# Optimization experiments

Measured on AMD Instinct MI355X. Metric: run time of the kernel, lower is better.

## Reference

```python
import jax, jax.numpy as jnp
import numpy as np
from jax import lax

B, T, V = 128, 256, 64
HF = 32   # MLP feature-imputation hidden
CTX = 32  # context hidden
HID = 64  # LSTM hidden


def _uniform(k, shape, fan):
    s = 1.0 / np.sqrt(fan)
    return jax.random.uniform(k, shape, jnp.float32, -s, s)


def setup_inputs():
    key = jax.random.key(0)
    ks = jax.random.split(key, 40)
    values = jax.random.normal(ks[0], (B, T, V), jnp.float32)
    masks = (jax.random.uniform(ks[1], (B, T, V)) > 0.3).astype(jnp.float32)
    deltas = jax.random.uniform(ks[2], (B, T, V), jnp.float32) * 5.0
    lengths = jax.random.randint(ks[3], (B,), T // 2, T + 1)
    min_vals = jnp.min(values, axis=1, keepdims=True)
    max_vals = jnp.max(values, axis=1, keepdims=True)
    D_in = 2 * V + 2 * CTX
    return dict(
        lengths=lengths, values=values, masks=masks, deltas=deltas,
        min_vals=min_vals, max_vals=max_vals,
        W_decay=_uniform(ks[4], (V, V), V), b_decay=_uniform(ks[5], (V,), V),
        W_feat=_uniform(ks[6], (V, HF, V), V), b_feat=_uniform(ks[7], (V, HF), V),
        W_nl1=_uniform(ks[8], (HF, HF), HF), b_nl1=_uniform(ks[9], (HF,), HF),
        W_nl2=_uniform(ks[10], (1, HF), HF), b_nl2=_uniform(ks[11], (1,), HF),
        Wc1=_uniform(ks[12], (2 * CTX, 3 * V + 1), 3 * V + 1), bc1=_uniform(ks[13], (2 * CTX,), 3 * V + 1),
        Wc2=_uniform(ks[14], (CTX, 2 * CTX), 2 * CTX), bc2=_uniform(ks[15], (CTX,), 2 * CTX),
        W_ih_g=_uniform(ks[16], (3 * CTX, 2 * V), CTX), W_hh_g=_uniform(ks[17], (3 * CTX, CTX), CTX),
        b_ih_g=_uniform(ks[18], (3 * CTX,), CTX), b_hh_g=_uniform(ks[19], (3 * CTX,), CTX),
        W_init=_uniform(ks[20], (2 * HID, 2 * CTX), 2 * CTX), b_init=_uniform(ks[21], (2 * HID,), 2 * CTX),
        W_ih_f=_uniform(ks[22], (4 * HID, D_in), HID), W_hh_f=_uniform(ks[23], (4 * HID, HID), HID),
        b_ih_f=_uniform(ks[24], (4 * HID,), HID), b_hh_f=_uniform(ks[25], (4 * HID,), HID),
        W_ih_b=_uniform(ks[26], (4 * HID, D_in), HID), W_hh_b=_uniform(ks[27], (4 * HID, HID), HID),
        b_ih_b=_uniform(ks[28], (4 * HID,), HID), b_hh_b=_uniform(ks[29], (4 * HID,), HID),
        W_ri=_uniform(ks[30], (V, 2 * HID), 2 * HID), b_ri=_uniform(ks[31], (V,), 2 * HID),
        W_fu=_uniform(ks[32], (V, 2 * V), 2 * V), b_fu=_uniform(ks[33], (V,), 2 * V),
    )


def _gru(x, h, Wih, Whh, bih, bhh):
    gi = x @ Wih.T + bih
    gh = h @ Whh.T + bhh
    ir, iz, inn = jnp.split(gi, 3, axis=-1)
    hr, hz, hn = jnp.split(gh, 3, axis=-1)
    r = jax.nn.sigmoid(ir + hr)
    z = jax.nn.sigmoid(iz + hz)
    n = jnp.tanh(inn + r * hn)
    return (1.0 - z) * n + z * h


def _lstm(x, h, c, Wih, Whh, bih, bhh):
    g = x @ Wih.T + bih + h @ Whh.T + bhh
    i, f, gg, o = jnp.split(g, 4, axis=-1)
    c = jax.nn.sigmoid(f) * c + jax.nn.sigmoid(i) * jnp.tanh(gg)
    h = jax.nn.sigmoid(o) * jnp.tanh(c)
    return h, c


def _forward(lengths, values, masks, deltas, min_vals, max_vals,
             W_decay, b_decay, W_feat, b_feat, W_nl1, b_nl1, W_nl2, b_nl2,
             Wc1, bc1, Wc2, bc2, W_ih_g, W_hh_g, b_ih_g, b_hh_g,
             W_init, b_init, W_ih_f, W_hh_f, b_ih_f, b_hh_f,
             W_ih_b, W_hh_b, b_ih_b, b_hh_b, W_ri, b_ri, W_fu, b_fu):
    Bb, Tt, Vv = values.shape
    lf = lengths.astype(jnp.float32)
    pad = (jnp.arange(Tt)[None, :] + 1 <= lengths[:, None]).astype(jnp.float32)  # [B,T]

    msum = masks.sum(axis=1)                       # [B,V] observation counts
    means = values.sum(axis=1) / msum
    var = ((values - means[:, None, :]) ** 2).sum(axis=1) / (msum - 1.0)
    stdev = jnp.sqrt(var)
    missing = 1.0 - msum / lf[:, None]
    stats = jnp.concatenate([lf[:, None], means, stdev, missing], axis=1)  # [B,3V+1]

    mmn = jnp.maximum(max_vals - min_vals, 1e-8)   # [B,1,V]
    nv = (values - min_vals) / mmn
    nmeans = (means - min_vals[:, 0, :]) / mmn[:, 0, :]

    # last-observation-carried-forward x_prime
    nv_tm = jnp.swapaxes(nv, 0, 1)   # [T,B,V]
    m_tm = jnp.swapaxes(masks, 0, 1)

    def pstep(xp, xm):
        x_prev, m_prev = xm
        xp = m_prev * x_prev + (1.0 - m_prev) * xp
        return xp, xp
    _, xp_rest = lax.scan(pstep, nv_tm[0], (nv_tm[:-1], m_tm[:-1]))
    x_prime = jnp.swapaxes(jnp.concatenate([nv_tm[:1], xp_rest], axis=0), 0, 1)

    # InputTemporalDecay: F.linear(d, W*I, b) == d * diag(W) + b
    gamma = jnp.exp(-jax.nn.relu(deltas * jnp.diag(W_decay) + b_decay))
    x_decay = gamma * x_prime + (1.0 - gamma) * nmeans[:, None, :]
    x_complete = masks * nv + (1.0 - masks) * x_decay

    # context vectors
    ctx_mlp = jax.nn.relu(stats @ Wc1.T + bc1) @ Wc2.T + bc2  # [B,CTX]
    x_rnn_tm = jnp.swapaxes(jnp.concatenate([x_complete, masks], axis=-1), 0, 1)  # [T,B,2V]
    pad_tm = jnp.swapaxes(pad, 0, 1)[:, :, None]
    h0 = jnp.zeros((Bb, W_hh_g.shape[1]), values.dtype)

    def gstep(carry, inp):
        h, hn = carry
        x_t, p_t = inp
        h = _gru(x_t, h, W_ih_g, W_hh_g, b_ih_g, b_hh_g)
        hn = p_t * h + (1.0 - p_t) * hn
        return (h, hn), None
    (_, ctx_rnn), _ = lax.scan(gstep, (h0, h0), (x_rnn_tm, pad_tm))
    context = jnp.concatenate([ctx_mlp, ctx_rnn], axis=1)  # [B,2*CTX]

    hinit = context @ W_init.T + b_init  # [B,2H]
    cinit = jnp.tanh(hinit)
    Hh = hinit.shape[1] // 2
    hf0, hb0 = hinit[:, :Hh], hinit[:, Hh:]
    cf0, cb0 = cinit[:, :Hh], cinit[:, Hh:]

    ctx_bt = jnp.broadcast_to(context[:, None, :], (Bb, Tt, context.shape[1]))
    rnn_in_tm = jnp.swapaxes(jnp.concatenate([x_complete, masks, ctx_bt], axis=-1), 0, 1)  # [T,B,D]

    def fstep(carry, x):
        h, c = _lstm(x, carry[0], carry[1], W_ih_f, W_hh_f, b_ih_f, b_hh_f)
        return (h, c), h
    _, hf_rest = lax.scan(fstep, (hf0, cf0), rnn_in_tm[:-1])
    hf_all = jnp.concatenate([hf0[None], hf_rest], axis=0)  # [T,B,H]

    def bstep(carry, x):
        h, c = _lstm(x, carry[0], carry[1], W_ih_b, W_hh_b, b_ih_b, b_hh_b)
        return (h, c), h
    _, hb_rest = lax.scan(bstep, (hb0, cb0), rnn_in_tm[1:][::-1])  # t = T-1 .. 1
    hb_all = jnp.concatenate([hb0[None], hb_rest], axis=0)[::-1]   # time-aligned

    h_cat = jnp.concatenate([hf_all, hb_all], axis=-1)  # [T,B,2H]
    rnn_imp = jnp.swapaxes(h_cat @ W_ri.T + b_ri, 0, 1)  # [B,T,V]

    # per-variable masked feature imputation (no self-connection)
    eye = jnp.eye(Vv, dtype=values.dtype)
    Wm = W_feat * (1.0 - eye[:, None, :])                 # [V,HF,V]
    hidden = jnp.einsum('btv,ghv->btgh', x_complete, Wm) + b_feat  # [B,T,V,HF]
    z = jax.nn.relu(hidden) @ W_nl1.T + b_nl1
    feat_imp = (jax.nn.relu(z) @ W_nl2.T + b_nl2)[..., 0]  # [B,T,V]

    beta = jax.nn.sigmoid(jnp.concatenate([gamma, masks], axis=-1) @ W_fu.T + b_fu)
    final_imp = beta * feat_imp + (1.0 - beta) * rnn_imp

    # unnormalize all three estimates; stack as [3,B,T,V]
    out = jnp.stack([rnn_imp, feat_imp, final_imp], axis=0) * mmn[None] + min_vals[None]
    return out


def reference(lengths, values, masks, deltas, min_vals, max_vals,
              W_decay, b_decay, W_feat, b_feat, W_nl1, b_nl1, W_nl2, b_nl2,
              Wc1, bc1, Wc2, bc2, W_ih_g, W_hh_g, b_ih_g, b_hh_g,
              W_init, b_init, W_ih_f, W_hh_f, b_ih_f, b_hh_f,
              W_ih_b, W_hh_b, b_ih_b, b_hh_b, W_ri, b_ri, W_fu, b_fu):
    return _forward(lengths, values, masks, deltas, min_vals, max_vals,
                    W_decay, b_decay, W_feat, b_feat, W_nl1, b_nl1, W_nl2, b_nl2,
                    Wc1, bc1, Wc2, bc2, W_ih_g, W_hh_g, b_ih_g, b_hh_g,
                    W_init, b_init, W_ih_f, W_hh_f, b_ih_f, b_hh_f,
                    W_ih_b, W_hh_b, b_ih_b, b_hh_b, W_ri, b_ri, W_fu, b_fu)
```

## Files before the change

### kernel.cpp

```cpp
#include <hip/hip_runtime.h>
#include <hip/hip_fp16.h>

static constexpr int NB = 128;
static constexpr int NT = 256;
static constexpr int NV = 64;
static constexpr int NBT = NB * NT;
static constexpr int NBTV = NBT * NV;

typedef __attribute__((ext_vector_type(8))) short short8;
typedef __attribute__((ext_vector_type(4))) float f32x4;
typedef __attribute__((ext_vector_type(4))) float fvec4;

__device__ __forceinline__ void wave_lds_fence() {
    __builtin_amdgcn_sched_barrier(0);
    asm volatile("s_waitcnt lgkmcnt(0)" ::: "memory");
    __builtin_amdgcn_sched_barrier(0);
}

__device__ __forceinline__ void block_sync_lds() {
    __builtin_amdgcn_sched_barrier(0);
    asm volatile("s_waitcnt lgkmcnt(0)" ::: "memory");
    __builtin_amdgcn_s_barrier();
    asm volatile("" ::: "memory");
    __builtin_amdgcn_sched_barrier(0);
}

__device__ __forceinline__ unsigned short f2bf(float x) {
    unsigned int u = __float_as_uint(x);
    return (unsigned short)((u + 0x7FFFu + ((u >> 16) & 1u)) >> 16);
}
__device__ __forceinline__ float bf2f(unsigned short b) {
    return __uint_as_float(((unsigned int)b) << 16);
}
__device__ __forceinline__ unsigned short f2h(float x) {
    union { _Float16 h; unsigned short u; } c; c.h = (_Float16)x; return c.u;
}
__device__ __forceinline__ float fsigm(float x) {
    return __builtin_amdgcn_rcpf(1.0f + __expf(-x));
}
__device__ __forceinline__ float ftanh(float x) {
    return 1.0f - 2.0f * __builtin_amdgcn_rcpf(1.0f + __expf(2.0f * x));
}

__device__ __forceinline__ short8 pack8(float4 a, float4 b) {
    short8 r;
    r[0] = (short)f2bf(a.x); r[1] = (short)f2bf(a.y); r[2] = (short)f2bf(a.z); r[3] = (short)f2bf(a.w);
    r[4] = (short)f2bf(b.x); r[5] = (short)f2bf(b.y); r[6] = (short)f2bf(b.z); r[7] = (short)f2bf(b.w);
    return r;
}

__device__ __forceinline__ void dot4(float4& acc, const float4 wv, const float4 xv) {
    acc.x = fmaf(wv.x, xv.x, acc.x);
    acc.y = fmaf(wv.y, xv.y, acc.y);
    acc.z = fmaf(wv.z, xv.z, acc.z);
    acc.w = fmaf(wv.w, xv.w, acc.w);
}

__global__ __launch_bounds__(256) void k_prep(
    const float* __restrict__ Wf, const float* __restrict__ Wihf,
    const float* __restrict__ Wihb, const float* __restrict__ Wihg,
    const float* __restrict__ Whhf, const float* __restrict__ Whhb,
    const float* __restrict__ Whhg, const float* __restrict__ Wri,
    const float* __restrict__ Wfu,
    unsigned short* __restrict__ wbf, float* __restrict__ wdiag,
    unsigned short* __restrict__ wgf, unsigned short* __restrict__ wgb,
    unsigned short* __restrict__ wgg,
    unsigned short* __restrict__ whhf_h, unsigned short* __restrict__ whhb_h,
    unsigned short* __restrict__ whhg_h,
    unsigned short* __restrict__ wri_bf, unsigned short* __restrict__ wfu_bf,
    const int* __restrict__ lengths, const float* __restrict__ values,
    const float* __restrict__ masks, const float* __restrict__ minv,
    const float* __restrict__ maxv, float* __restrict__ stats,
    float* __restrict__ mmn_ws, float* __restrict__ nmeans_ws) {
    __shared__ float red[3][4][64];
    int bx = blockIdx.x;
    if (bx < 512) {
        int i = bx * 256 + threadIdx.x;
        if (i < NV * 32 * NV) wbf[i] = f2bf(Wf[i]);
        if (i < 2048) wdiag[i] = bf2f(f2bf(Wf[i * 64 + (i >> 5)]));
        if (i < 32768) {
            int n = i >> 7, k = i & 127;
            wgf[i] = f2bf(Wihf[n * 192 + k]);
            wgb[i] = f2bf(Wihb[n * 192 + k]);
        }
        if (i < 12288) wgg[i] = f2bf(Wihg[i]);
        if (i < 16384) { whhf_h[i] = f2h(Whhf[i]); whhb_h[i] = f2h(Whhb[i]); }
        if (i < 3072) whhg_h[i] = f2h(Whhg[i]);
        if (i < 8192) { wri_bf[i] = f2bf(Wri[i]); wfu_bf[i] = f2bf(Wfu[i]); }
    } else {
        int b = bx - 512; int tid = threadIdx.x;
        int v = tid & 63; int tc = tid >> 6;
        const float* vp = values + (size_t)b * NT * NV;
        const float* mp = masks + (size_t)b * NT * NV;
        float sv = 0.f, sq = 0.f, sm = 0.f;
        for (int t = tc; t < NT; t += 4) {
            float x = vp[t * NV + v]; float m = mp[t * NV + v];
            sv += x; sq += x * x; sm += m;
        }
        red[0][tc][v] = sv; red[1][tc][v] = sq; red[2][tc][v] = sm;
        __syncthreads();
        if (tc == 0) {
            sv = red[0][0][v] + red[0][1][v] + red[0][2][v] + red[0][3][v];
            sq = red[1][0][v] + red[1][1][v] + red[1][2][v] + red[1][3][v];
            sm = red[2][0][v] + red[2][1][v] + red[2][2][v] + red[2][3][v];
            float mean = sv / sm;
            float var = (sq - 2.0f * mean * sv + (float)NT * mean * mean) / (sm - 1.0f);
            var = fmaxf(var, 0.0f);
            float sd = sqrtf(var);
            float lf = (float)lengths[b];
            float miss = 1.0f - sm / lf;
            float mn = minv[b * NV + v]; float mx = maxv[b * NV + v];
            float mm = fmaxf(mx - mn, 1e-8f);
            float* st = stats + b * 256;
            if (v == 0) st[0] = lf;
            st[1 + v] = mean; st[65 + v] = sd; st[129 + v] = miss;
            mmn_ws[b * NV + v] = mm;
            nmeans_ws[b * NV + v] = (mean - mn) / mm;
        }
    }
}

__global__ __launch_bounds__(256) void k_fill(
    const float* __restrict__ values, const float* __restrict__ masks,
    const float* __restrict__ deltas, const float* __restrict__ minv,
    const float* __restrict__ Wd, const float* __restrict__ bd,
    const float* __restrict__ mmn_ws, const float* __restrict__ nmeans_ws,
    float* __restrict__ xcomp, float* __restrict__ gam) {
    int b = blockIdx.x; int tid = threadIdx.x;
    int v = tid & 63; int tc = tid >> 6;
    float mn = minv[b * NV + v];
    float mm = mmn_ws[b * NV + v];
    float nmean = nmeans_ws[b * NV + v];
    float wd = Wd[v * NV + v], bdv = bd[v];
    size_t base = (size_t)b * NT * NV + v;
    __shared__ float lastv[4][64];
    __shared__ int hasf[4][64];
    __shared__ float nv0s[64];
    int t0 = tc * 64;
    float last = 0.f; int has = 0;
    for (int t = t0; t < t0 + 64; t++) {
        float val = values[base + (size_t)t * NV];
        float m = masks[base + (size_t)t * NV];
        float nv = (val - mn) / mm;
        if (m != 0.f) { last = nv; has = 1; }
        if (tc == 0 && t == 0) nv0s[v] = nv;
    }
    lastv[tc][v] = last; hasf[tc][v] = has;
    __syncthreads();
    float xp = nv0s[v];
    for (int q = tc - 1; q >= 0; q--) {
        if (hasf[q][v]) { xp = lastv[q][v]; break; }
    }
    for (int t = t0; t < t0 + 64; t++) {
        size_t i = base + (size_t)t * NV;
        float val = values[i], m = masks[i], d = deltas[i];
        float nv = (val - mn) / mm;
        float g = expf(-fmaxf(fmaf(d, wd, bdv), 0.0f));
        float xd = g * xp + (1.0f - g) * nmean;
        float xc = m * nv + (1.0f - m) * xd;
        xcomp[i] = xc; gam[i] = g;
        xp = (m != 0.f) ? nv : xp;
    }
}

__global__ __launch_bounds__(256) void k_gates_g(
    const float* __restrict__ xcomp, const float* __restrict__ masks,
    const unsigned short* __restrict__ wgg, const float* __restrict__ bihg,
    float* __restrict__ gg) {
    int wave = threadIdx.x >> 6, lane = threadIdx.x & 63;
    int bt0 = blockIdx.x * 64 + wave * 16;
    int r = lane & 15, kc = lane >> 4;
    const float* xr = xcomp + (size_t)(bt0 + r) * NV + kc * 8;
    const float* mr = masks + (size_t)(bt0 + r) * NV + kc * 8;
    short8 af0 = pack8(*(const float4*)(xr), *(const float4*)(xr + 4));
    short8 af1 = pack8(*(const float4*)(xr + 32), *(const float4*)(xr + 36));
    short8 af2 = pack8(*(const float4*)(mr), *(const float4*)(mr + 4));
    short8 af3 = pack8(*(const float4*)(mr + 32), *(const float4*)(mr + 36));
    #pragma unroll 3
    for (int nt = 0; nt < 6; nt++) {
        const unsigned short* w = wgg + (size_t)(nt * 16 + r) * 128 + kc * 8;
        float bias = bihg[nt * 16 + r];
        f32x4 acc = {bias, bias, bias, bias};
        acc = __builtin_amdgcn_mfma_f32_16x16x32_bf16(af0, *(const short8*)(w), acc, 0, 0, 0);
        acc = __builtin_amdgcn_mfma_f32_16x16x32_bf16(af1, *(const short8*)(w + 32), acc, 0, 0, 0);
        acc = __builtin_amdgcn_mfma_f32_16x16x32_bf16(af2, *(const short8*)(w + 64), acc, 0, 0, 0);
        acc = __builtin_amdgcn_mfma_f32_16x16x32_bf16(af3, *(const short8*)(w + 96), acc, 0, 0, 0);
        #pragma unroll
        for (int i = 0; i < 4; i++)
            gg[(size_t)(bt0 + kc * 4 + i) * 96 + nt * 16 + r] = acc[i];
    }
}

#define GRU_STEP(T, GIN) { \
    const int t_ = (T); const int p_ = t_ & 1; \
    int4 raw_[4]; \
    const int4* hp_ = (const int4*)hsg[g][s]; \
    _Pragma("unroll") for (int q = 0; q < 4; q++) raw_[q] = hp_[q]; \
    const __half2* hhv_ = (const __half2*)raw_; \
    __half2 a0_ = zh2, a1_ = zh2, a2_ = zh2, a3_ = zh2; \
    _Pragma("unroll") for (int q = 0; q < 16; q += 4) { \
        a0_ = __hfma2(w2[q],     hhv_[q],     a0_); \
        a1_ = __hfma2(w2[q + 1], hhv_[q + 1], a1_); \
        a2_ = __hfma2(w2[q + 2], hhv_[q + 2], a2_); \
        a3_ = __hfma2(w2[q + 3], hhv_[q + 3], a3_); } \
    __half2 sA_ = __hadd2(__hadd2(a0_, a1_), __hadd2(a2_, a3_)); \
    float d_ = __low2float(sA_) + __high2float(sA_); \
    if (g < 2) { \
        gexg[p_][s][n][g] = GIN + bh + d_; \
    } else { \
        gexg[p_][s][n][2] = bh + d_; \
        gexg[p_][s][n][3] = GIN; \
    } \
    block_sync_lds(); \
    float qx_ = gexg[p_][s][n][0], qy_ = gexg[p_][s][n][1]; \
    float qz_ = gexg[p_][s][n][2], qw_ = gexg[p_][s][n][3]; \
    float rr_ = fsigm(qx_); \
    float zz_ = fsigm(qy_); \
    float nn_ = ftanh(qw_ + rr_ * qz_); \
    float h_ = (1.f - zz_) * nn_ + zz_ * hprev; \
    hprev = h_; \
    if (t_ < len) hn = h_; \
    hsg[g][s][n] = f2h(h_); \
    wave_lds_fence(); \
}

#define FEAT_BODY(BT0) { \
    int bt0 = (BT0); \
    int r = lane & 15, kc = lane >> 4; \
    unsigned short* hbw = hbs[wave]; \
    float* lx = ldsx[wave]; \
    float* flw = fls[wave]; \
    short8 a0, a1; \
    { \
        const float* xr = xcomp + (size_t)(bt0 + r) * NV + kc * 8; \
        a0 = pack8(*(const float4*)(xr), *(const float4*)(xr + 4)); \
        a1 = pack8(*(const float4*)(xr + 32), *(const float4*)(xr + 36)); \
    } \
    { \
        int gc0 = kc * 16; \
        const float* xr2 = xcomp + (size_t)(bt0 + r) * NV + gc0; \
        _Pragma("unroll") for (int e = 0; e < 16; e += 4) { \
            float4 p = *(const float4*)(xr2 + e); \
            lx[(gc0 + e + 0) * 16 + r] = bf2f(f2bf(p.x)); \
            lx[(gc0 + e + 1) * 16 + r] = bf2f(f2bf(p.y)); \
            lx[(gc0 + e + 2) * 16 + r] = bf2f(f2bf(p.z)); \
            lx[(gc0 + e + 3) * 16 + r] = bf2f(f2bf(p.w)); \
        } \
    } \
    short8 wb0, wb1; \
    { \
        const float* w = Wnl1 + r * 32 + kc * 8; \
        wb0 = pack8(*(const float4*)w, *(const float4*)(w + 4)); \
        const float* w2p = Wnl1 + (16 + r) * 32 + kc * 8; \
        wb1 = pack8(*(const float4*)w2p, *(const float4*)(w2p + 4)); \
    } \
    float b0i[4], b1i[4], w2a[4], w2b[4]; \
    _Pragma("unroll") for (int i = 0; i < 4; i++) { \
        b0i[i] = bnl1[kc * 4 + i]; \
        b1i[i] = bnl1[16 + kc * 4 + i]; \
        w2a[i] = Wnl2[kc * 4 + i]; \
        w2b[i] = Wnl2[16 + kc * 4 + i]; \
    } \
    float bn2 = bnl2[0]; \
    __builtin_amdgcn_wave_barrier(); \
    _Pragma("unroll 2") for (int g = 0; g < 64; g++) { \
        __builtin_amdgcn_wave_barrier(); \
        float xv[4]; \
        _Pragma("unroll") for (int i = 0; i < 4; i++) xv[i] = lx[g * 16 + kc * 4 + i]; \
        _Pragma("unroll") for (int f = 0; f < 2; f++) { \
            int n0 = g * 32 + f * 16; \
            const unsigned short* wrow = wbf + (size_t)(n0 + r) * 64; \
            short8 b0 = *(const short8*)(wrow + kc * 8); \
            short8 b1 = *(const short8*)(wrow + 32 + kc * 8); \
            f32x4 acc = {0.f, 0.f, 0.f, 0.f}; \
            acc = __builtin_amdgcn_mfma_f32_16x16x32_bf16(a0, b0, acc, 0, 0, 0); \
            acc = __builtin_amdgcn_mfma_f32_16x16x32_bf16(a1, b1, acc, 0, 0, 0); \
            int n = n0 + r; \
            float wd = wdiag[n], bs = bfeat[n]; \
            _Pragma("unroll") for (int i = 0; i < 4; i++) { \
                float h = acc[i] - xv[i] * wd + bs; \
                h = fmaxf(h, 0.0f); \
                hbw[(kc * 4 + i) * 32 + f * 16 + r] = f2bf(h); \
            } \
        } \
        __builtin_amdgcn_wave_barrier(); \
        short8 ah = *(const short8*)(hbw + r * 32 + kc * 8); \
        f32x4 zt0 = {0.f, 0.f, 0.f, 0.f}, zt1 = {0.f, 0.f, 0.f, 0.f}; \
        zt0 = __builtin_amdgcn_mfma_f32_16x16x32_bf16(wb0, ah, zt0, 0, 0, 0); \
        zt1 = __builtin_amdgcn_mfma_f32_16x16x32_bf16(wb1, ah, zt1, 0, 0, 0); \
        float p = 0.f; \
        _Pragma("unroll") for (int i = 0; i < 4; i++) { \
            p = fmaf(fmaxf(zt0[i] + b0i[i], 0.0f), w2a[i], p); \
            p = fmaf(fmaxf(zt1[i] + b1i[i], 0.0f), w2b[i], p); \
        } \
        p += __shfl_xor(p, 16, 64); \
        p += __shfl_xor(p, 32, 64); \
        if (lane < 16) flw[lane * 65 + g] = p + bn2; \
    } \
    __builtin_amdgcn_wave_barrier(); \
    _Pragma("unroll") for (int q = 0; q < 16; q++) \
        feat_out[(size_t)(bt0 + q) * NV + lane] = flw[q * 65 + lane]; \
}

__global__ __launch_bounds__(256, 1) void k_mid(
    const float* __restrict__ gg_t, const int* __restrict__ lengths,
    const unsigned short* __restrict__ whhg_h, const float* __restrict__ bhh,
    float* __restrict__ ctx,
    const float* __restrict__ stats, const float* __restrict__ Wc1,
    const float* __restrict__ bc1, const float* __restrict__ Wc2,
    const float* __restrict__ bc2,
    const float* __restrict__ xcomp, const float* __restrict__ masks,
    const unsigned short* __restrict__ wbf,
    const float* __restrict__ wdiag, const float* __restrict__ bfeat,
    const float* __restrict__ Wnl1, const float* __restrict__ bnl1,
    const float* __restrict__ Wnl2, const float* __restrict__ bnl2,
    float* __restrict__ feat_out,
    const unsigned short* __restrict__ wgf, const unsigned short* __restrict__ wgb,
    float* __restrict__ gf, float* __restrict__ gb) {
    __shared__ __align__(16) unsigned short hsg[3][2][32];
    __shared__ __align__(16) float gexg[2][2][32][5];
    __shared__ __align__(16) float ss[193];
    __shared__ float h1[64];
    __shared__ __align__(16) unsigned short hbs[4][16 * 32];
    __shared__ __align__(16) float ldsx[4][64 * 16];
    __shared__ __align__(16) float fls[4][16 * 65];

    int bx = blockIdx.x;
    int tid = threadIdx.x;

    if (bx < 64) {
        int b0 = bx * 2;
        int g = tid >> 6;
        int lane = tid & 63;
        int s = lane >> 5, n = lane & 31;
        if (g == 3) {
            for (int t = 0; t < NT; t++) block_sync_lds();
            return;
        }
        int b = b0 + s;
        const __half2 zh2 = __float2half2_rn(0.f);
        int4 w4[4];
        {
            const int4* wp = (const int4*)(whhg_h + (size_t)(g * 32 + n) * 32);
            #pragma unroll
            for (int q = 0; q < 4; q++) w4[q] = wp[q];
        }
        const __half2* w2 = (const __half2*)w4;
        float bh = bhh[g * 32 + n];
        int len = lengths[b];
        float hprev = 0.f, hn = 0.f;
        hsg[g][s][n] = f2h(0.f);
        const float* gbase = gg_t + (size_t)b * NT * 96;
        #define GGIDX(T) ((size_t)(T) * 96 + g * 32 + n)
        float gi0 = gbase[GGIDX(0)];
        float gi1 = gbase[GGIDX(1)];
        float gi2 = gbase[GGIDX(2)];
        float gi3 = gbase[GGIDX(3)];
        wave_lds_fence();
        for (int t = 0; t < 252; t += 4) {
            GRU_STEP(t, gi0)
            gi0 = gbase[GGIDX(t + 4)];
            GRU_STEP(t + 1, gi1)
            gi1 = gbase[GGIDX(t + 5)];
            GRU_STEP(t + 2, gi2)
            gi2 = gbase[GGIDX(t + 6)];
            GRU_STEP(t + 3, gi3)
            gi3 = gbase[GGIDX(t + 7)];
        }
        GRU_STEP(252, gi0)
        GRU_STEP(253, gi1)
        GRU_STEP(254, gi2)
        GRU_STEP(255, gi3)
        #undef GGIDX
        if (g == 0) ctx[(b0 + s) * 64 + 32 + n] = hn;
    } else if (bx < 192) {
        if (tid >= 64) return;
        int b = bx - 64;
        ss[tid] = stats[b * 256 + tid];
        ss[64 + tid] = stats[b * 256 + 64 + tid];
        ss[128 + tid] = stats[b * 256 + 128 + tid];
        if (tid == 0) ss[192] = stats[b * 256 + 192];
        wave_lds_fence();
        float acc = bc1[tid];
        const float* w = Wc1 + (size_t)tid * 193;
        for (int k = 0; k < 193; k++) acc = fmaf(w[k], ss[k], acc);
        h1[tid] = fmaxf(acc, 0.f);
        wave_lds_fence();
        if (tid < 32) {
            float a = bc2[tid];
            const float* w2 = Wc2 + tid * 64;
            for (int k = 0; k < 64; k++) a = fmaf(w2[k], h1[k], a);
            ctx[b * 64 + tid] = a;
        }
    } else if (bx < 448) {
        int wave = tid >> 6; int lane = tid & 63;
        FEAT_BODY((bx - 192) * 64 + wave * 16)
    } else {
        int wave = tid >> 6, lane = tid & 63;
        int bt0 = (bx - 448) * 64 + wave * 16;
        int r = lane & 15, kc = lane >> 4;
        const float* xr = xcomp + (size_t)(bt0 + r) * NV + kc * 8;
        const float* mr = masks + (size_t)(bt0 + r) * NV + kc * 8;
        short8 af0 = pack8(*(const float4*)(xr), *(const float4*)(xr + 4));
        short8 af1 = pack8(*(const float4*)(xr + 32), *(const float4*)(xr + 36));
        short8 af2 = pack8(*(const float4*)(mr), *(const float4*)(mr + 4));
        short8 af3 = pack8(*(const float4*)(mr + 32), *(const float4*)(mr + 36));
        #pragma unroll 4
        for (int nt = 0; nt < 16; nt++) {
            const unsigned short* w = wgf + (size_t)(nt * 16 + r) * 128 + kc * 8;
            f32x4 acc = {0.f, 0.f, 0.f, 0.f};
            acc = __builtin_amdgcn_mfma_f32_16x16x32_bf16(af0, *(const short8*)(w), acc, 0, 0, 0);
            acc = __builtin_amdgcn_mfma_f32_16x16x32_bf16(af1, *(const short8*)(w + 32), acc, 0, 0, 0);
            acc = __builtin_amdgcn_mfma_f32_16x16x32_bf16(af2, *(const short8*)(w + 64), acc, 0, 0, 0);
            acc = __builtin_amdgcn_mfma_f32_16x16x32_bf16(af3, *(const short8*)(w + 96), acc, 0, 0, 0);
            int col = nt * 16 + r, g = col >> 6, n = col & 63;
            #pragma unroll
            for (int i = 0; i < 4; i++)
                gf[((size_t)(bt0 + kc * 4 + i) * 64 + n) * 4 + g] = acc[i];
        }
        #pragma unroll 4
        for (int nt = 0; nt < 16; nt++) {
            const unsigned short* w = wgb + (size_t)(nt * 16 + r) * 128 + kc * 8;
            f32x4 acc = {0.f, 0.f, 0.f, 0.f};
            acc = __builtin_amdgcn_mfma_f32_16x16x32_bf16(af0, *(const short8*)(w), acc, 0, 0, 0);
            acc = __builtin_amdgcn_mfma_f32_16x16x32_bf16(af1, *(const short8*)(w + 32), acc, 0, 0, 0);
            acc = __builtin_amdgcn_mfma_f32_16x16x32_bf16(af2, *(const short8*)(w + 64), acc, 0, 0, 0);
            acc = __builtin_amdgcn_mfma_f32_16x16x32_bf16(af3, *(const short8*)(w + 96), acc, 0, 0, 0);
            int col = nt * 16 + r, g = col >> 6, n = col & 63;
            #pragma unroll
            for (int i = 0; i < 4; i++)
                gb[((size_t)(bt0 + kc * 4 + i) * 64 + n) * 4 + g] = acc[i];
        }
    }
}

#define LSTM_STEP(S, GIN) { \
    const int s_ = (S); const int p_ = s_ & 1; \
    int4 raw_[8]; \
    const int4* hp_ = (const int4*)hs[g]; \
    _Pragma("unroll") for (int q = 0; q < 8; q++) raw_[q] = hp_[q]; \
    const __half2* hhv_ = (const __half2*)raw_; \
    __half2 a0_ = zh2, a1_ = zh2, a2_ = zh2, a3_ = zh2; \
    _Pragma("unroll") for (int q = 0; q < 32; q += 4) { \
        a0_ = __hfma2(w2[q],     hhv_[q],     a0_); \
        a1_ = __hfma2(w2[q + 1], hhv_[q + 1], a1_); \
        a2_ = __hfma2(w2[q + 2], hhv_[q + 2], a2_); \
        a3_ = __hfma2(w2[q + 3], hhv_[q + 3], a3_); } \
    __half2 sA_ = __hadd2(__hadd2(a0_, a1_), __hadd2(a2_, a3_)); \
    float d_ = __low2float(sA_) + __high2float(sA_); \
    gex[p_][n][g] = GIN + ctg + d_; \
    block_sync_lds(); \
    float qx_ = gex[p_][n][0], qy_ = gex[p_][n][1]; \
    float qz_ = gex[p_][n][2], qw_ = gex[p_][n][3]; \
    float ii_ = fsigm(qx_); \
    float ff_ = fsigm(qy_); \
    float gv_ = ftanh(qz_); \
    float oo_ = fsigm(qw_); \
    c = ff_ * c + ii_ * gv_; \
    float hv_ = oo_ * ftanh(c); \
    if (g == 0) { \
        int tout_ = dir ? (NT - 2 - s_) : (s_ + 1); \
        hall[((size_t)b * NT + tout_) * NV + n] = hv_; \
    } \
    hs[g][n] = f2h(hv_); \
    wave_lds_fence(); \
}

__global__ __launch_bounds__(256, 1) void k_lstm(
    const float* __restrict__ gf, const float* __restrict__ gb,
    const float* __restrict__ ctx,
    const unsigned short* __restrict__ whhf_h, const unsigned short* __restrict__ whhb_h,
    const float* __restrict__ Wihf, const float* __restrict__ Wihb,
    const float* __restrict__ bihf, const float* __restrict__ bhhf,
    const float* __restrict__ bihb, const float* __restrict__ bhhb,
    const float* __restrict__ Wini, const float* __restrict__ bini,
    float* __restrict__ out0, float* __restrict__ out1,
    const float* __restrict__ xcomp, const unsigned short* __restrict__ wbf,
    const float* __restrict__ wdiag, const float* __restrict__ bfeat,
    const float* __restrict__ Wnl1, const float* __restrict__ bnl1,
    const float* __restrict__ Wnl2, const float* __restrict__ bnl2,
    float* __restrict__ feat_out) {
    __shared__ __align__(16) unsigned short hs[4][64];
    __shared__ __align__(16) float gex[2][64][5];
    __shared__ __align__(16) float sctx[64];
    __shared__ __align__(16) float sh0[64];
    __shared__ __align__(16) unsigned short hbs[4][16 * 32];
    __shared__ __align__(16) float ldsx[4][64 * 16];
    __shared__ __align__(16) float fls[4][16 * 65];

    int bx = blockIdx.x;
    int tid = threadIdx.x;

    if (bx >= 256) {
        int wave = tid >> 6; int lane = tid & 63;
        FEAT_BODY((bx - 256) * 64 + 16384 + wave * 16)
        return;
    }

    int dir = bx >> 7; int b = bx & 127;
    int g = tid >> 6;
    int n = tid & 63;
    const float* gates = dir ? gb : gf;
    const unsigned short* wsrc = dir ? whhb_h : whhf_h;
    float* hall = dir ? out1 : out0;
    const __half2 zh2 = __float2half2_rn(0.f);
    int4 w4[8];
    {
        const int4* wp = (const int4*)(wsrc + (size_t)(g * 64 + n) * 64);
        #pragma unroll
        for (int q = 0; q < 8; q++) w4[q] = wp[q];
    }
    const __half2* w2 = (const __half2*)w4;
    size_t gbase = (size_t)b * NT * 256;
    #define GIDX(S) (gbase + (size_t)(dir ? (NT - 1 - (S)) : (S)) * 256 + n * 4 + g)
    float gi0 = gates[GIDX(0)];
    float gi1 = gates[GIDX(1)];
    float gi2 = gates[GIDX(2)];
    float gi3 = gates[GIDX(3)];
    if (tid < 64) sctx[tid] = ctx[b * 64 + tid];
    __syncthreads();
    float ctg;
    {
        const float4* wc = (const float4*)((dir ? Wihb : Wihf) + (size_t)tid * 192 + 128);
        float bias = dir ? (bihb[tid] + bhhb[tid]) : (bihf[tid] + bhhf[tid]);
        const float4* c4 = (const float4*)sctx;
        float4 a = {0, 0, 0, 0};
        #pragma unroll
        for (int q = 0; q < 16; q++) dot4(a, wc[q], c4[q]);
        ctg = bias + a.x + a.y + a.z + a.w;
    }
    if (tid < 64) {
        const float4* wi = (const float4*)(Wini + (size_t)(dir * 64 + tid) * 64);
        const float4* c4 = (const float4*)sctx;
        float4 a = {0, 0, 0, 0};
        #pragma unroll
        for (int q = 0; q < 16; q++) dot4(a, wi[q], c4[q]);
        sh0[tid] = bini[dir * 64 + tid] + a.x + a.y + a.z + a.w;
    }
    __syncthreads();
    float c;
    {
        float h0 = sh0[n];
        c = ftanh(h0);
        hs[g][n] = f2h(h0);
        if (g == 0) {
            int t0 = dir ? (NT - 1) : 0;
            hall[((size_t)b * NT + t0) * NV + n] = h0;
        }
    }
    wave_lds_fence();
    for (int sx = 0; sx < 252; sx += 4) {
        LSTM_STEP(sx, gi0)
        gi0 = gates[GIDX(sx + 4)];
        LSTM_STEP(sx + 1, gi1)
        gi1 = gates[GIDX(sx + 5)];
        LSTM_STEP(sx + 2, gi2)
        gi2 = gates[GIDX(sx + 6)];
        LSTM_STEP(sx + 3, gi3)
        gi3 = gates[GIDX(sx + 7)];
    }
    LSTM_STEP(252, gi0)
    LSTM_STEP(253, gi1)
    LSTM_STEP(254, gi2)
    #undef GIDX
}

__global__ __launch_bounds__(256) void k_post(
    const float* __restrict__ gam, const float* __restrict__ masks,
    const unsigned short* __restrict__ wri_bf, const unsigned short* __restrict__ wfu_bf,
    const float* __restrict__ bri, const float* __restrict__ bfu,
    const float* __restrict__ mmn_ws, const float* __restrict__ minv,
    float* out0, float* out1, float* out2) {
    int wave = threadIdx.x >> 6, lane = threadIdx.x & 63;
    int bt0 = blockIdx.x * 64 + wave * 16;
    int r = lane & 15, kc = lane >> 4;
    int b = bt0 >> 8;
    const float* h0r = out0 + (size_t)(bt0 + r) * NV + kc * 8;
    const float* h1r = out1 + (size_t)(bt0 + r) * NV + kc * 8;
    const float* gr  = gam  + (size_t)(bt0 + r) * NV + kc * 8;
    const float* mr  = masks + (size_t)(bt0 + r) * NV + kc * 8;
    short8 A0 = pack8(*(const float4*)(h0r), *(const float4*)(h0r + 4));
    short8 A1 = pack8(*(const float4*)(h0r + 32), *(const float4*)(h0r + 36));
    short8 A2 = pack8(*(const float4*)(h1r), *(const float4*)(h1r + 4));
    short8 A3 = pack8(*(const float4*)(h1r + 32), *(const float4*)(h1r + 36));
    short8 G0 = pack8(*(const float4*)(gr), *(const float4*)(gr + 4));
    short8 G1 = pack8(*(const float4*)(gr + 32), *(const float4*)(gr + 36));
    short8 M0 = pack8(*(const float4*)(mr), *(const float4*)(mr + 4));
    short8 M1 = pack8(*(const float4*)(mr + 32), *(const float4*)(mr + 36));
    #pragma unroll
    for (int nt = 0; nt < 4; nt++) {
        int n = nt * 16 + r;
        const unsigned short* wr = wri_bf + (size_t)n * 128 + kc * 8;
        const unsigned short* wf = wfu_bf + (size_t)n * 128 + kc * 8;
        float bi = bri[n], bf_ = bfu[n];
        f32x4 racc = {bi, bi, bi, bi};
        f32x4 bacc = {bf_, bf_, bf_, bf_};
        racc = __builtin_amdgcn_mfma_f32_16x16x32_bf16(A0, *(const short8*)(wr), racc, 0, 0, 0);
        racc = __builtin_amdgcn_mfma_f32_16x16x32_bf16(A1, *(const short8*)(wr + 32), racc, 0, 0, 0);
        racc = __builtin_amdgcn_mfma_f32_16x16x32_bf16(A2, *(const short8*)(wr + 64), racc, 0, 0, 0);
        racc = __builtin_amdgcn_mfma_f32_16x16x32_bf16(A3, *(const short8*)(wr + 96), racc, 0, 0, 0);
        bacc = __builtin_amdgcn_mfma_f32_16x16x32_bf16(G0, *(const short8*)(wf), bacc, 0, 0, 0);
        bacc = __builtin_amdgcn_mfma_f32_16x16x32_bf16(G1, *(const short8*)(wf + 32), bacc, 0, 0, 0);
        bacc = __builtin_amdgcn_mfma_f32_16x16x32_bf16(M0, *(const short8*)(wf + 64), bacc, 0, 0, 0);
        bacc = __builtin_amdgcn_mfma_f32_16x16x32_bf16(M1, *(const short8*)(wf + 96), bacc, 0, 0, 0);
        float mm = mmn_ws[b * NV + n], mn = minv[b * NV + n];
        #pragma unroll
        for (int i = 0; i < 4; i++) {
            int row = bt0 + kc * 4 + i;
            size_t idx = (size_t)row * NV + n;
            float rn = racc[i];
            float beta = fsigm(bacc[i]);
            float ft = out2[idx];
            float fin = beta * ft + (1.0f - beta) * rn;
            out0[idx] = fmaf(rn, mm, mn);
            out1[idx] = fmaf(ft, mm, mn);
            out2[idx] = fmaf(fin, mm, mn);
        }
    }
}

extern "C" void kernel_launch(void* const* d_in, const int* in_sizes, int n_in,
                              void* d_out, int out_size, void* d_ws, size_t ws_size,
                              hipStream_t stream) {
    const int*   lengths  = (const int*)d_in[0];
    const float* values   = (const float*)d_in[1];
    const float* masks    = (const float*)d_in[2];
    const float* deltas   = (const float*)d_in[3];
    const float* min_vals = (const float*)d_in[4];
    const float* max_vals = (const float*)d_in[5];
    const float* W_decay  = (const float*)d_in[6];
    const float* b_decay  = (const float*)d_in[7];
    const float* W_feat   = (const float*)d_in[8];
    const float* b_feat   = (const float*)d_in[9];
    const float* W_nl1    = (const float*)d_in[10];
    const float* b_nl1    = (const float*)d_in[11];
    const float* W_nl2    = (const float*)d_in[12];
    const float* b_nl2    = (const float*)d_in[13];
    const float* Wc1      = (const float*)d_in[14];
    const float* bc1      = (const float*)d_in[15];
    const float* Wc2      = (const float*)d_in[16];
    const float* bc2      = (const float*)d_in[17];
    const float* W_ih_g   = (const float*)d_in[18];
    const float* W_hh_g   = (const float*)d_in[19];
    const float* b_ih_g   = (const float*)d_in[20];
    const float* b_hh_g   = (const float*)d_in[21];
    const float* W_init   = (const float*)d_in[22];
    const float* b_init   = (const float*)d_in[23];
    const float* W_ih_f   = (const float*)d_in[24];
    const float* W_hh_f   = (const float*)d_in[25];
    const float* b_ih_f   = (const float*)d_in[26];
    const float* b_hh_f   = (const float*)d_in[27];
    const float* W_ih_b   = (const float*)d_in[28];
    const float* W_hh_b   = (const float*)d_in[29];
    const float* b_ih_b   = (const float*)d_in[30];
    const float* b_hh_b   = (const float*)d_in[31];
    const float* W_ri     = (const float*)d_in[32];
    const float* b_ri     = (const float*)d_in[33];
    const float* W_fu     = (const float*)d_in[34];
    const float* b_fu     = (const float*)d_in[35];

    float* ws = (float*)d_ws;
    float* xcomp  = ws;
    float* gam    = ws + 2097152;
    unsigned short* wri_bf = (unsigned short*)(ws + 4194304);
    unsigned short* wfu_bf = (unsigned short*)(ws + 4198400);
    float* stats  = ws + 6291456;
    float* mmn    = ws + 6324224;
    float* nmeans = ws + 6332416;
    float* ctx    = ws + 6340608;
    unsigned short* wbf = (unsigned short*)(ws + 6365184);
    float* wdiag  = ws + 6430720;
    unsigned short* wgf = (unsigned short*)(ws + 6432768);
    unsigned short* wgb = (unsigned short*)(ws + 6449152);
    unsigned short* wgg = (unsigned short*)(ws + 6465536);
    unsigned short* whhf_h = (unsigned short*)(ws + 6471680);
    unsigned short* whhb_h = (unsigned short*)(ws + 6479872);
    unsigned short* whhg_h = (unsigned short*)(ws + 6488064);
    float* gates_f = ws + 6555136;
    float* gates_b = ws + 14943744;
    float* gates_g = ws + 23332352;

    float* out0 = (float*)d_out;
    float* out1 = out0 + NBTV;
    float* out2 = out0 + 2 * NBTV;

    k_prep<<<640, 256, 0, stream>>>(W_feat, W_ih_f, W_ih_b, W_ih_g, W_hh_f, W_hh_b, W_hh_g,
                                    W_ri, W_fu,
                                    wbf, wdiag, wgf, wgb, wgg, whhf_h, whhb_h, whhg_h,
                                    wri_bf, wfu_bf,
                                    lengths, values, masks, min_vals, max_vals, stats, mmn, nmeans);
    k_fill<<<NB, 256, 0, stream>>>(values, masks, deltas, min_vals, W_decay, b_decay, mmn, nmeans, xcomp, gam);
    k_gates_g<<<NBT / 64, 256, 0, stream>>>(xcomp, masks, wgg, b_ih_g, gates_g);
    k_mid<<<960, 256, 0, stream>>>(gates_g, lengths, whhg_h, b_hh_g, ctx,
                                   stats, Wc1, bc1, Wc2, bc2,
                                   xcomp, masks, wbf, wdiag, b_feat, W_nl1, b_nl1, W_nl2, b_nl2, out2,
                                   wgf, wgb, gates_f, gates_b);
    k_lstm<<<512, 256, 0, stream>>>(gates_f, gates_b, ctx, whhf_h, whhb_h,
                                    W_ih_f, W_ih_b, b_ih_f, b_hh_f, b_ih_b, b_hh_b,
                                    W_init, b_init, out0, out1,
                                    xcomp, wbf, wdiag, b_feat, W_nl1, b_nl1, W_nl2, b_nl2, out2);
    k_post<<<NBT / 64, 256, 0, stream>>>(gam, masks, wri_bf, wfu_bf, b_ri, b_fu, mmn, min_vals,
                                         out0, out1, out2);
}
```

Baseline: 285.4 us.

## Fold per-batch stats into fill kernel and move feature MLP into LSTM launch

Moves the per-batch mean/std/missing-rate reduction out of the prep kernel into the forward-fill kernel, which already reads values and masks, so those arrays are read once and a launch region is dropped. Normalization is now applied after the reduction, using shared-memory mm/nmean. All feature-imputation MLP blocks move from the mid kernel into the LSTM kernel, where they run alongside the latency-bound recurrent blocks instead of competing with the gate-projection work. The risk is that the LSTM launch gets longer if the extra feature blocks delay the recurrent blocks or fail to fill idle CUs.

Result: slower. 295.0 us (+3.4%).

```diff
diff --git a/kernel.cpp b/kernel.cpp
--- a/kernel.cpp
+++ b/kernel.cpp
@@ -67,89 +67,79 @@
     unsigned short* __restrict__ wgg,
     unsigned short* __restrict__ whhf_h, unsigned short* __restrict__ whhb_h,
     unsigned short* __restrict__ whhg_h,
-    unsigned short* __restrict__ wri_bf, unsigned short* __restrict__ wfu_bf,
-    const int* __restrict__ lengths, const float* __restrict__ values,
-    const float* __restrict__ masks, const float* __restrict__ minv,
-    const float* __restrict__ maxv, float* __restrict__ stats,
-    float* __restrict__ mmn_ws, float* __restrict__ nmeans_ws) {
-    __shared__ float red[3][4][64];
-    int bx = blockIdx.x;
-    if (bx < 512) {
-        int i = bx * 256 + threadIdx.x;
-        if (i < NV * 32 * NV) wbf[i] = f2bf(Wf[i]);
-        if (i < 2048) wdiag[i] = bf2f(f2bf(Wf[i * 64 + (i >> 5)]));
-        if (i < 32768) {
-            int n = i >> 7, k = i & 127;
-            wgf[i] = f2bf(Wihf[n * 192 + k]);
-            wgb[i] = f2bf(Wihb[n * 192 + k]);
-        }
-        if (i < 12288) wgg[i] = f2bf(Wihg[i]);
-        if (i < 16384) { whhf_h[i] = f2h(Whhf[i]); whhb_h[i] = f2h(Whhb[i]); }
-        if (i < 3072) whhg_h[i] = f2h(Whhg[i]);
-        if (i < 8192) { wri_bf[i] = f2bf(Wri[i]); wfu_bf[i] = f2bf(Wfu[i]); }
-    } else {
-        int b = bx - 512; int tid = threadIdx.x;
-        int v = tid & 63; int tc = tid >> 6;
-        const float* vp = values + (size_t)b * NT * NV;
-        const float* mp = masks + (size_t)b * NT * NV;
-        float sv = 0.f, sq = 0.f, sm = 0.f;
-        for (int t = tc; t < NT; t += 4) {
-            float x = vp[t * NV + v]; float m = mp[t * NV + v];
-            sv += x; sq += x * x; sm += m;
-        }
-        red[0][tc][v] = sv; red[1][tc][v] = sq; red[2][tc][v] = sm;
-        __syncthreads();
-        if (tc == 0) {
-            sv = red[0][0][v] + red[0][1][v] + red[0][2][v] + red[0][3][v];
-            sq = red[1][0][v] + red[1][1][v] + red[1][2][v] + red[1][3][v];
-            sm = red[2][0][v] + red[2][1][v] + red[2][2][v] + red[2][3][v];
-            float mean = sv / sm;
-            float var = (sq - 2.0f * mean * sv + (float)NT * mean * mean) / (sm - 1.0f);
-            var = fmaxf(var, 0.0f);
-            float sd = sqrtf(var);
-            float lf = (float)lengths[b];
-            float miss = 1.0f - sm / lf;
-            float mn = minv[b * NV + v]; float mx = maxv[b * NV + v];
-            float mm = fmaxf(mx - mn, 1e-8f);
-            float* st = stats + b * 256;
-            if (v == 0) st[0] = lf;
-            st[1 + v] = mean; st[65 + v] = sd; st[129 + v] = miss;
-            mmn_ws[b * NV + v] = mm;
-            nmeans_ws[b * NV + v] = (mean - mn) / mm;
-        }
-    }
+    unsigned short* __restrict__ wri_bf, unsigned short* __restrict__ wfu_bf) {
+    int i = blockIdx.x * 256 + threadIdx.x;
+    if (i < NV * 32 * NV) wbf[i] = f2bf(Wf[i]);
+    if (i < 2048) wdiag[i] = bf2f(f2bf(Wf[i * 64 + (i >> 5)]));
+    if (i < 32768) {
+        int n = i >> 7, k = i & 127;
+        wgf[i] = f2bf(Wihf[n * 192 + k]);
+        wgb[i] = f2bf(Wihb[n * 192 + k]);
+    }
+    if (i < 12288) wgg[i] = f2bf(Wihg[i]);
+    if (i < 16384) { whhf_h[i] = f2h(Whhf[i]); whhb_h[i] = f2h(Whhb[i]); }
+    if (i < 3072) whhg_h[i] = f2h(Whhg[i]);
+    if (i < 8192) { wri_bf[i] = f2bf(Wri[i]); wfu_bf[i] = f2bf(Wfu[i]); }
 }
 
 __global__ __launch_bounds__(256) void k_fill(
+    const int* __restrict__ lengths,
     const float* __restrict__ values, const float* __restrict__ masks,
     const float* __restrict__ deltas, const float* __restrict__ minv,
+    const float* __restrict__ maxv,
     const float* __restrict__ Wd, const float* __restrict__ bd,
-    const float* __restrict__ mmn_ws, const float* __restrict__ nmeans_ws,
+    float* __restrict__ stats,
+    float* __restrict__ mmn_ws, float* __restrict__ nmeans_ws,
     float* __restrict__ xcomp, float* __restrict__ gam) {
     int b = blockIdx.x; int tid = threadIdx.x;
     int v = tid & 63; int tc = tid >> 6;
     float mn = minv[b * NV + v];
-    float mm = mmn_ws[b * NV + v];
-    float nmean = nmeans_ws[b * NV + v];
-    float wd = Wd[v * NV + v], bdv = bd[v];
     size_t base = (size_t)b * NT * NV + v;
+    __shared__ float red[3][4][64];
     __shared__ float lastv[4][64];
     __shared__ int hasf[4][64];
     __shared__ float nv0s[64];
+    __shared__ float smm[64], snm[64];
     int t0 = tc * 64;
+    float sv = 0.f, sq = 0.f, sm = 0.f;
     float last = 0.f; int has = 0;
     for (int t = t0; t < t0 + 64; t++) {
         float val = values[base + (size_t)t * NV];
         float m = masks[base + (size_t)t * NV];
-        float nv = (val - mn) / mm;
-        if (m != 0.f) { last = nv; has = 1; }
-        if (tc == 0 && t == 0) nv0s[v] = nv;
-    }
+        sv += val; sq += val * val; sm += m;
+        if (m != 0.f) { last = val; has = 1; }
+        if (tc == 0 && t == 0) nv0s[v] = val;
+    }
+    red[0][tc][v] = sv; red[1][tc][v] = sq; red[2][tc][v] = sm;
     lastv[tc][v] = last; hasf[tc][v] = has;
     __syncthreads();
-    float xp = nv0s[v];
+    if (tc == 0) {
+        sv = red[0][0][v] + red[0][1][v] + red[0][2][v] + red[0][3][v];
+        sq = red[1][0][v] + red[1][1][v] + red[1][2][v] + red[1][3][v];
+        sm = red[2][0][v] + red[2][1][v] + red[2][2][v] + red[2][3][v];
+        float mean = sv / sm;
+        float var = (sq - 2.0f * mean * sv + (float)NT * mean * mean) / (sm - 1.0f);
+        var = fmaxf(var, 0.0f);
+        float sd = sqrtf(var);
+        float lf = (float)lengths[b];
+        float miss = 1.0f - sm / lf;
+        float mx = maxv[b * NV + v];
+        float mm = fmaxf(mx - mn, 1e-8f);
+        float* st = stats + b * 256;
+        if (v == 0) st[0] = lf;
+        st[1 + v] = mean; st[65 + v] = sd; st[129 + v] = miss;
+        float nmean = (mean - mn) / mm;
+        mmn_ws[b * NV + v] = mm;
+        nmeans_ws[b * NV + v] = nmean;
+        smm[v] = mm; snm[v] = nmean;
+    }
+    __syncthreads();
+    float mm = smm[v];
+    float nmean = snm[v];
+    float wd = Wd[v * NV + v], bdv = bd[v];
+    float xp = (nv0s[v] - mn) / mm;
     for (int q = tc - 1; q >= 0; q--) {
-        if (hasf[q][v]) { xp = lastv[q][v]; break; }
+        if (hasf[q][v]) { xp = (lastv[q][v] - mn) / mm; break; }
     }
     for (int t = t0; t < t0 + 64; t++) {
         size_t i = base + (size_t)t * NV;
@@ -310,20 +300,12 @@
     const float* __restrict__ bc1, const float* __restrict__ Wc2,
     const float* __restrict__ bc2,
     const float* __restrict__ xcomp, const float* __restrict__ masks,
-    const unsigned short* __restrict__ wbf,
-    const float* __restrict__ wdiag, const float* __restrict__ bfeat,
-    const float* __restrict__ Wnl1, const float* __restrict__ bnl1,
-    const float* __restrict__ Wnl2, const float* __restrict__ bnl2,
-    float* __restrict__ feat_out,
     const unsigned short* __restrict__ wgf, const unsigned short* __restrict__ wgb,
     float* __restrict__ gf, float* __restrict__ gb) {
     __shared__ __align__(16) unsigned short hsg[3][2][32];
     __shared__ __align__(16) float gexg[2][2][32][5];
     __shared__ __align__(16) float ss[193];
     __shared__ float h1[64];
-    __shared__ __align__(16) unsigned short hbs[4][16 * 32];
-    __shared__ __align__(16) float ldsx[4][64 * 16];
-    __shared__ __align__(16) float fls[4][16 * 65];
 
     int bx = blockIdx.x;
     int tid = threadIdx.x;
@@ -392,12 +374,9 @@
             for (int k = 0; k < 64; k++) a = fmaf(w2[k], h1[k], a);
             ctx[b * 64 + tid] = a;
         }
-    } else if (bx < 448) {
-        int wave = tid >> 6; int lane = tid & 63;
-        FEAT_BODY((bx - 192) * 64 + wave * 16)
     } else {
         int wave = tid >> 6, lane = tid & 63;
-        int bt0 = (bx - 448) * 64 + wave * 16;
+        int bt0 = (bx - 192) * 64 + wave * 16;
         int r = lane & 15, kc = lane >> 4;
         const float* xr = xcomp + (size_t)(bt0 + r) * NV + kc * 8;
         const float* mr = masks + (size_t)(bt0 + r) * NV + kc * 8;
@@ -493,7 +472,7 @@
 
     if (bx >= 256) {
         int wave = tid >> 6; int lane = tid & 63;
-        FEAT_BODY((bx - 256) * 64 + 16384 + wave * 16)
+        FEAT_BODY((bx - 256) * 64 + wave * 16)
         return;
     }
 
@@ -684,18 +663,17 @@
     float* out1 = out0 + NBTV;
     float* out2 = out0 + 2 * NBTV;
 
-    k_prep<<<640, 256, 0, stream>>>(W_feat, W_ih_f, W_ih_b, W_ih_g, W_hh_f, W_hh_b, W_hh_g,
+    k_prep<<<512, 256, 0, stream>>>(W_feat, W_ih_f, W_ih_b, W_ih_g, W_hh_f, W_hh_b, W_hh_g,
                                     W_ri, W_fu,
                                     wbf, wdiag, wgf, wgb, wgg, whhf_h, whhb_h, whhg_h,
-                                    wri_bf, wfu_bf,
-                                    lengths, values, masks, min_vals, max_vals, stats, mmn, nmeans);
-    k_fill<<<NB, 256, 0, stream>>>(values, masks, deltas, min_vals, W_decay, b_decay, mmn, nmeans, xcomp, gam);
+                                    wri_bf, wfu_bf);
+    k_fill<<<NB, 256, 0, stream>>>(lengths, values, masks, deltas, min_vals, max_vals,
+                                   W_decay, b_decay, stats, mmn, nmeans, xcomp, gam);
     k_gates_g<<<NBT / 64, 256, 0, stream>>>(xcomp, masks, wgg, b_ih_g, gates_g);
-    k_mid<<<960, 256, 0, stream>>>(gates_g, lengths, whhg_h, b_hh_g, ctx,
+    k_mid<<<704, 256, 0, stream>>>(gates_g, lengths, whhg_h, b_hh_g, ctx,
                                    stats, Wc1, bc1, Wc2, bc2,
-                                   xcomp, masks, wbf, wdiag, b_feat, W_nl1, b_nl1, W_nl2, b_nl2, out2,
-                                   wgf, wgb, gates_f, gates_b);
-    k_lstm<<<512, 256, 0, stream>>>(gates_f, gates_b, ctx, whhf_h, whhb_h,
+                                   xcomp, masks, wgf, wgb, gates_f, gates_b);
+    k_lstm<<<768, 256, 0, stream>>>(gates_f, gates_b, ctx, whhf_h, whhb_h,
                                     W_ih_f, W_ih_b, b_ih_f, b_hh_f, b_ih_b, b_hh_b,
                                     W_init, b_init, out0, out1,
                                     xcomp, wbf, wdiag, b_feat, W_nl1, b_nl1, W_nl2, b_nl2, out2);
```
